# Kernel tuning notes

Measured on AMD Instinct MI355X. Metric: run time of the kernel, lower is better.

## Reference

```python
import jax, jax.numpy as jnp
import numpy as np

D_MODEL = 1024
N_HEADS = 16
D_K = D_MODEL // N_HEADS


def setup_inputs() -> dict:
    key = jax.random.key(0)
    kx, kq, kk, kv, ko = jax.random.split(key, 5)
    s = 1.0 / np.sqrt(D_MODEL)
    return {
        "x": jax.random.normal(kx, (4, 2048, D_MODEL), dtype=jnp.float32),
        "W_q": jax.random.normal(kq, (D_MODEL, D_MODEL), dtype=jnp.float32) * s,
        "W_k": jax.random.normal(kk, (D_MODEL, D_MODEL), dtype=jnp.float32) * s,
        "W_v": jax.random.normal(kv, (D_MODEL, D_MODEL), dtype=jnp.float32) * s,
        "W_o": jax.random.normal(ko, (D_MODEL, D_MODEL), dtype=jnp.float32) * s,
    }


def reference(x, W_q, W_k, W_v, W_o):
    B, S, _ = x.shape
    # torch nn.Linear computes x @ W.T; our W_* stored as [out, in]-equivalent square,
    # use plain x @ W (equivalent parameterization for a random weight).
    def split_heads(t):  # [B,S,D] -> [B,H,S,d_k]
        return t.reshape(B, S, N_HEADS, D_K).transpose(0, 2, 1, 3)

    Q = split_heads(x @ W_q)
    K = split_heads(x @ W_k)
    V = split_heads(x @ W_v)
    scale = 1.0 / np.sqrt(D_K).astype(np.float32)
    scores = jnp.einsum('bhqd,bhkd->bhqk', Q, K) * scale  # [B,H,S,S]
    causal_mask = jnp.tril(jnp.ones((S, S), dtype=bool))  # True = keep
    scores = jnp.where(causal_mask, scores, jnp.float32(-jnp.inf))
    attn = jax.nn.softmax(scores, axis=-1)
    out = jnp.einsum('bhqk,bhkd->bhqd', attn, V)  # [B,H,S,d_k]
    out = out.transpose(0, 2, 1, 3).reshape(B, S, D_MODEL)
    return out @ W_o
```

## Files before the change

### kernel.cpp

```cpp
#include <hip/hip_runtime.h>
#include <hip/hip_bf16.h>
#include <stdint.h>

#define B_SZ 4
#define SEQ 2048
#define DM 1024
#define NH 16
#define DK 64
#define BH (B_SZ * NH)
#define M_TOT (B_SZ * SEQ)

typedef unsigned short u16;
typedef u16 u16x8 __attribute__((ext_vector_type(8)));
typedef __bf16 bf16x8 __attribute__((ext_vector_type(8)));
typedef float f32x4 __attribute__((ext_vector_type(4)));

__device__ __forceinline__ u16 f2bf(float f) {
    union { float f; uint32_t u; } v; v.f = f;
    uint32_t u = v.u;
    return (u16)((u + 0x7FFFu + ((u >> 16) & 1u)) >> 16);
}

__device__ __forceinline__ u16 f2bf_trunc(float f) {
    union { float f; uint32_t u; } v; v.f = f;
    return (u16)(v.u >> 16);
}

__device__ __forceinline__ f32x4 mfma16(u16x8 a, u16x8 b, f32x4 c) {
    return __builtin_amdgcn_mfma_f32_16x16x32_bf16(
        __builtin_bit_cast(bf16x8, a), __builtin_bit_cast(bf16x8, b), c, 0, 0, 0);
}

__device__ __forceinline__ void gload16_lds(const void* g, void* l) {
    __builtin_amdgcn_global_load_lds(
        (const __attribute__((address_space(1))) void*)(uintptr_t)g,
        (__attribute__((address_space(3))) void*)(uintptr_t)l, 16, 0, 0);
}

__global__ void cvt_bf16_kernel(const float* __restrict__ in, u16* __restrict__ out, int n4) {
    int i = blockIdx.x * blockDim.x + threadIdx.x;
    if (i < n4) {
        float4 v = ((const float4*)in)[i];
        ushort4 o;
        o.x = f2bf(v.x); o.y = f2bf(v.y); o.z = f2bf(v.z); o.w = f2bf(v.w);
        ((ushort4*)out)[i] = o;
    }
}

__global__ void transpose_w_kernel(const float* __restrict__ W0, const float* __restrict__ W1,
                                   u16* __restrict__ Wt) {
    __shared__ u16 tile[32][33];
    int bx = blockIdx.x, by = blockIdx.y, z = blockIdx.z;
    const float* W = z ? W1 : W0;
    u16* Wd = Wt + (size_t)z * DM * DM;
    int t = threadIdx.x;
    for (int i = 0; i < 4; i++) {
        int idx = t + i * 256;
        int r = idx >> 5, c = idx & 31;
        tile[r][c] = f2bf(W[(by * 32 + r) * DM + bx * 32 + c]);
    }
    __syncthreads();
    for (int i = 0; i < 4; i++) {
        int idx = t + i * 256;
        int r2 = idx >> 5, c2 = idx & 31;
        Wd[(bx * 32 + r2) * DM + by * 32 + c2] = tile[c2][r2];
    }
}

template <int AFP32, int MODE>
__global__ __launch_bounds__(256, 2) void gemm128(
    const void* __restrict__ Ain, const u16* __restrict__ Bt,
    void* __restrict__ C0p, void* __restrict__ C1p, float scale0) {
    __shared__ u16 As[128][32];
    __shared__ u16 Bs[128][32];
    const int K = DM;
    int m0 = blockIdx.x * 128;
    int n0 = blockIdx.y * 128;
    int tid = threadIdx.x;
    int lane = tid & 63, wave = tid >> 6;
    int quad = lane >> 4, l15 = lane & 15;
    int wm = wave >> 1, wn = wave & 1;

    f32x4 acc[4][4];
    for (int i = 0; i < 4; i++)
        for (int j = 0; j < 4; j++) acc[i][j] = f32x4{0.f, 0.f, 0.f, 0.f};

    int rS = lane >> 2;
    int cS = (lane & 3) * 8;

    for (int k0 = 0; k0 < K; k0 += 32) {
        __syncthreads();
        if (AFP32) {
            const float* A = (const float*)Ain;
            for (int i = 0; i < 4; i++) {
                int idx = tid + i * 256;
                int r = idx >> 3, c = (idx & 7) * 4;
                float4 v = *(const float4*)(&A[(size_t)(m0 + r) * K + k0 + c]);
                ushort4 o;
                o.x = f2bf(v.x); o.y = f2bf(v.y); o.z = f2bf(v.z); o.w = f2bf(v.w);
                *(ushort4*)(&As[r][c]) = o;
            }
        } else {
            const u16* A = (const u16*)Ain;
            const u16* ga = &A[(size_t)(m0 + wave * 32 + rS) * K + k0 + cS];
            gload16_lds(ga, &As[wave * 32][0]);
            gload16_lds(ga + (size_t)16 * K, &As[wave * 32 + 16][0]);
        }
        {
            const u16* gb = &Bt[(size_t)(n0 + wave * 32 + rS) * K + k0 + cS];
            gload16_lds(gb, &Bs[wave * 32][0]);
            gload16_lds(gb + (size_t)16 * K, &Bs[wave * 32 + 16][0]);
        }
        __syncthreads();
        u16x8 af[4], bfv[4];
        for (int mt = 0; mt < 4; mt++)
            af[mt] = *(const u16x8*)(&As[wm * 64 + mt * 16 + l15][quad * 8]);
        for (int nt = 0; nt < 4; nt++)
            bfv[nt] = *(const u16x8*)(&Bs[wn * 64 + nt * 16 + l15][quad * 8]);
        for (int mt = 0; mt < 4; mt++)
            for (int nt = 0; nt < 4; nt++)
                acc[mt][nt] = mfma16(af[mt], bfv[nt], acc[mt][nt]);
    }

    for (int mt = 0; mt < 4; mt++)
        for (int nt = 0; nt < 4; nt++)
            for (int r = 0; r < 4; r++) {
                int m = m0 + wm * 64 + mt * 16 + quad * 4 + r;
                int n = n0 + wn * 64 + nt * 16 + l15;
                float v = acc[mt][nt][r];
                if (MODE == 0) {
                    v *= (n < 1024) ? scale0 : 1.0f;
                    u16* C = (n < 1024) ? (u16*)C0p : (u16*)C1p;
                    int ne = n & 1023;
                    int b = m >> 11, s = m & 2047;
                    int h = ne >> 6, d = ne & 63;
                    C[(((size_t)(b * NH + h) * SEQ) + s) * DK + d] = f2bf(v);
                } else if (MODE == 1) {
                    ((float*)C0p)[(size_t)m * DM + n] = v;
                } else {
                    int b = m >> 11, s = m & 2047;
                    int h = n >> 6, d = n & 63;
                    ((u16*)C0p)[(((size_t)(b * NH + h) * DK) + d) * SEQ + s] = f2bf(v);
                }
            }
}

__global__ __launch_bounds__(256, 6) void attn_kernel(
    const u16* __restrict__ Qb, const u16* __restrict__ Kb,
    const u16* __restrict__ Vtb, u16* __restrict__ AOb) {
    __shared__ u16 Kl[2][64][32];
    __shared__ u16 Vl[2][64][32];
    __shared__ u16 Pl[64][68];

    int bh = blockIdx.x;
    int qs = 31 - blockIdx.y;
    int q0 = qs * 64;
    int tid = threadIdx.x, lane = tid & 63, wave = tid >> 6;
    int quad = lane >> 4, l15 = lane & 15;
    int b = bh >> 4, h = bh & 15;

    const u16* Qg = Qb + (size_t)bh * SEQ * DK;
    const u16* Kg = Kb + (size_t)bh * SEQ * DK;
    const u16* Vg = Vtb + (size_t)bh * DK * SEQ;

    int rS = lane >> 2;
    int cS = (lane & 3) * 8;
    u16* Pw = &Pl[wave * 16][0];

    u16x8 aq[2];
    for (int kc = 0; kc < 2; kc++)
        aq[kc] = *(const u16x8*)(
            &Qg[(size_t)(q0 + wave * 16 + l15) * DK + kc * 32 + quad * 8]);

    float lsum[4];
    f32x4 O[4];
    for (int r = 0; r < 4; r++) lsum[r] = 0.f;
    for (int nt = 0; nt < 4; nt++) O[nt] = f32x4{0.f, 0.f, 0.f, 0.f};

    for (int kt = 0; kt <= qs; kt++) {
        int k0 = kt * 64;
        __syncthreads();
        {
            const u16* gk = &Kg[(size_t)(k0 + wave * 16 + rS) * DK + cS];
            gload16_lds(gk, &Kl[0][wave * 16][0]);
            gload16_lds(gk + 32, &Kl[1][wave * 16][0]);
            const u16* gv = &Vg[(size_t)(wave * 16 + rS) * SEQ + k0 + cS];
            gload16_lds(gv, &Vl[0][wave * 16][0]);
            gload16_lds(gv + 32, &Vl[1][wave * 16][0]);
        }
        __syncthreads();

        f32x4 sc[4];
        for (int nt = 0; nt < 4; nt++) {
            u16x8 b0 = *(const u16x8*)(&Kl[0][nt * 16 + l15][quad * 8]);
            u16x8 b1 = *(const u16x8*)(&Kl[1][nt * 16 + l15][quad * 8]);
            f32x4 z = f32x4{0.f, 0.f, 0.f, 0.f};
            z = mfma16(aq[0], b0, z);
            z = mfma16(aq[1], b1, z);
            sc[nt] = z;
        }
        if (kt == qs) {
            for (int nt = 0; nt < 4; nt++)
                for (int r = 0; r < 4; r++) {
                    int qq = wave * 16 + quad * 4 + r;
                    int kk = nt * 16 + l15;
                    float e = exp2f(sc[nt][r]);
                    float pv = (kk <= qq) ? e : 0.f;
                    sc[nt][r] = pv;
                    lsum[r] += pv;
                }
        } else {
            for (int nt = 0; nt < 4; nt++)
                for (int r = 0; r < 4; r++) {
                    float pv = exp2f(sc[nt][r]);
                    sc[nt][r] = pv;
                    lsum[r] += pv;
                }
        }
        for (int nt = 0; nt < 4; nt++)
            for (int r = 0; r < 4; r++)
                Pw[(size_t)(quad * 4 + r) * 68 + nt * 16 + l15] = f2bf_trunc(sc[nt][r]);
        u16x8 ap0 = *(const u16x8*)(&Pw[(size_t)l15 * 68 + quad * 8]);
        u16x8 ap1 = *(const u16x8*)(&Pw[(size_t)l15 * 68 + 32 + quad * 8]);
        for (int nt = 0; nt < 4; nt++) {
            u16x8 b0 = *(const u16x8*)(&Vl[0][nt * 16 + l15][quad * 8]);
            u16x8 b1 = *(const u16x8*)(&Vl[1][nt * 16 + l15][quad * 8]);
            O[nt] = mfma16(ap0, b0, O[nt]);
            O[nt] = mfma16(ap1, b1, O[nt]);
        }
    }

    for (int r = 0; r < 4; r++) {
        float s = lsum[r];
        for (int off = 1; off < 16; off <<= 1) s += __shfl_xor(s, off, 64);
        float inv = 1.0f / s;
        int q = q0 + wave * 16 + quad * 4 + r;
        for (int nt = 0; nt < 4; nt++) {
            int d = nt * 16 + l15;
            AOb[((size_t)(b * SEQ + q)) * DM + h * DK + d] = f2bf(O[nt][r] * inv);
        }
    }
}

extern "C" void kernel_launch(void* const* d_in, const int* in_sizes, int n_in,
                              void* d_out, int out_size, void* d_ws, size_t ws_size,
                              hipStream_t stream) {
    const float* x = (const float*)d_in[0];
    const float* Wq = (const float*)d_in[1];
    const float* Wk = (const float*)d_in[2];
    const float* Wv = (const float*)d_in[3];
    const float* Wo = (const float*)d_in[4];
    float* out = (float*)d_out;

    const size_t HALF = (size_t)M_TOT * DM * 2;
    char* S0 = (char*)d_ws;
    char* S1 = (char*)d_ws + HALF;
    char* D0 = (char*)d_out;
    char* D1 = (char*)d_out + HALF;

    u16* xb  = (u16*)S0;
    u16* Qb  = (u16*)S1;
    u16* Kb  = (u16*)D1;
    u16* Vt  = (u16*)D0;
    u16* AOb = (u16*)S0;
    u16* wqk = (u16*)D0;
    u16* wvt = (u16*)S0;
    u16* wot = (u16*)S1;

    const float cscale = 0.125f * 1.44269504088896f;
    dim3 tg2(32, 32, 2);
    dim3 tg1(32, 32, 1);
    dim3 gg(M_TOT / 128, DM / 128);

    int n4 = M_TOT * DM / 4;
    cvt_bf16_kernel<<<n4 / 256, 256, 0, stream>>>(x, xb, n4);

    transpose_w_kernel<<<tg2, 256, 0, stream>>>(Wq, Wk, wqk);
    dim3 gqk(M_TOT / 128, 2048 / 128);
    gemm128<0, 0><<<gqk, 256, 0, stream>>>(xb, wqk, (void*)Qb, (void*)Kb, cscale);

    transpose_w_kernel<<<tg1, 256, 0, stream>>>(Wv, Wv, wvt);
    gemm128<1, 2><<<gg, 256, 0, stream>>>(x, wvt, (void*)Vt, (void*)Vt, 1.0f);

    dim3 ag(BH, 32);
    attn_kernel<<<ag, 256, 0, stream>>>(Qb, Kb, Vt, AOb);

    transpose_w_kernel<<<tg1, 256, 0, stream>>>(Wo, Wo, wot);
    gemm128<0, 1><<<gg, 256, 0, stream>>>(AOb, wot, (void*)out, (void*)out, 1.0f);
}
```

Measured before the change: 294.7 us.

## Double-buffer K/V tiles in attention with XOR-swizzled LDS layout

The attention kernel now prefetches the next K/V tile into a second LDS buffer while computing on the current one, replacing the two barriers per iteration with one. The LDS tile layout changes to full 64-wide rows with an XOR swizzle on 8-element chunks, so the global-to-LDS copies and the MFMA operand reads avoid bank conflicts. Launch bounds drop from 6 to 3 blocks per CU because of the larger LDS footprint, which lowers occupancy in exchange for overlapping memory latency.

```diff
diff --git a/kernel.cpp b/kernel.cpp
--- a/kernel.cpp
+++ b/kernel.cpp
@@ -145,11 +145,11 @@
             }
 }
 
-__global__ __launch_bounds__(256, 6) void attn_kernel(
+__global__ __launch_bounds__(256, 3) void attn_kernel(
     const u16* __restrict__ Qb, const u16* __restrict__ Kb,
     const u16* __restrict__ Vtb, u16* __restrict__ AOb) {
-    __shared__ u16 Kl[2][64][32];
-    __shared__ u16 Vl[2][64][32];
+    __shared__ u16 Kl[2][64][64];
+    __shared__ u16 Vl[2][64][64];
     __shared__ u16 Pl[64][68];
 
     int bh = blockIdx.x;
@@ -163,8 +163,9 @@
     const u16* Kg = Kb + (size_t)bh * SEQ * DK;
     const u16* Vg = Vtb + (size_t)bh * DK * SEQ;
 
-    int rS = lane >> 2;
-    int cS = (lane & 3) * 8;
+    int rw = lane >> 3;
+    int gsw = (lane & 7) ^ rw;
+    int sw8 = l15 & 15 & 7;
     u16* Pw = &Pl[wave * 16][0];
 
     u16x8 aq[2];
@@ -177,23 +178,33 @@
     for (int r = 0; r < 4; r++) lsum[r] = 0.f;
     for (int nt = 0; nt < 4; nt++) O[nt] = f32x4{0.f, 0.f, 0.f, 0.f};
 
+    {
+        const u16* gk = &Kg[(size_t)(wave * 16 + rw) * DK + gsw * 8];
+        gload16_lds(gk, &Kl[0][wave * 16][0]);
+        gload16_lds(gk + 8 * DK, &Kl[0][wave * 16 + 8][0]);
+        const u16* gv = &Vg[(size_t)(wave * 16 + rw) * SEQ + gsw * 8];
+        gload16_lds(gv, &Vl[0][wave * 16][0]);
+        gload16_lds(gv + 8 * SEQ, &Vl[0][wave * 16 + 8][0]);
+    }
+    __syncthreads();
+
+    int buf = 0;
     for (int kt = 0; kt <= qs; kt++) {
-        int k0 = kt * 64;
-        __syncthreads();
-        {
-            const u16* gk = &Kg[(size_t)(k0 + wave * 16 + rS) * DK + cS];
-            gload16_lds(gk, &Kl[0][wave * 16][0]);
-            gload16_lds(gk + 32, &Kl[1][wave * 16][0]);
-            const u16* gv = &Vg[(size_t)(wave * 16 + rS) * SEQ + k0 + cS];
-            gload16_lds(gv, &Vl[0][wave * 16][0]);
-            gload16_lds(gv + 32, &Vl[1][wave * 16][0]);
-        }
-        __syncthreads();
+        if (kt < qs) {
+            int k0n = (kt + 1) * 64;
+            const u16* gk = &Kg[(size_t)(k0n + wave * 16 + rw) * DK + gsw * 8];
+            gload16_lds(gk, &Kl[buf ^ 1][wave * 16][0]);
+            gload16_lds(gk + 8 * DK, &Kl[buf ^ 1][wave * 16 + 8][0]);
+            const u16* gv = &Vg[(size_t)(wave * 16 + rw) * SEQ + k0n + gsw * 8];
+            gload16_lds(gv, &Vl[buf ^ 1][wave * 16][0]);
+            gload16_lds(gv + 8 * SEQ, &Vl[buf ^ 1][wave * 16 + 8][0]);
+        }
 
         f32x4 sc[4];
         for (int nt = 0; nt < 4; nt++) {
-            u16x8 b0 = *(const u16x8*)(&Kl[0][nt * 16 + l15][quad * 8]);
-            u16x8 b1 = *(const u16x8*)(&Kl[1][nt * 16 + l15][quad * 8]);
+            const u16* kr = &Kl[buf][nt * 16 + l15][0];
+            u16x8 b0 = *(const u16x8*)(kr + (quad ^ sw8) * 8);
+            u16x8 b1 = *(const u16x8*)(kr + ((4 + quad) ^ sw8) * 8);
             f32x4 z = f32x4{0.f, 0.f, 0.f, 0.f};
             z = mfma16(aq[0], b0, z);
             z = mfma16(aq[1], b1, z);
@@ -223,11 +234,14 @@
         u16x8 ap0 = *(const u16x8*)(&Pw[(size_t)l15 * 68 + quad * 8]);
         u16x8 ap1 = *(const u16x8*)(&Pw[(size_t)l15 * 68 + 32 + quad * 8]);
         for (int nt = 0; nt < 4; nt++) {
-            u16x8 b0 = *(const u16x8*)(&Vl[0][nt * 16 + l15][quad * 8]);
-            u16x8 b1 = *(const u16x8*)(&Vl[1][nt * 16 + l15][quad * 8]);
+            const u16* vr = &Vl[buf][nt * 16 + l15][0];
+            u16x8 b0 = *(const u16x8*)(vr + (quad ^ sw8) * 8);
+            u16x8 b1 = *(const u16x8*)(vr + ((4 + quad) ^ sw8) * 8);
             O[nt] = mfma16(ap0, b0, O[nt]);
             O[nt] = mfma16(ap1, b1, O[nt]);
         }
+        __syncthreads();
+        buf ^= 1;
     }
 
     for (int r = 0; r < 4; r++) {
```

After: 291.5 us. Within noise of the previous version (-1.1%).
